# Kernel optimization log

Measured on AMD Instinct MI355X. Metric: run time of the kernel, lower is better.

The kernel has to match this reference:

```python
import jax, jax.numpy as jnp
import numpy as np

# Problem sizes
N = 131072      # total nodes (B graphs x 256 nodes)
E = 1048576     # total edges (avg degree 8)
V = 30000       # vocab
D = 128         # emb_size
H = 128         # hidden_size
T = 4           # num edge types; edge_to_id['ne'] == 0
L = 2           # num RGCN layers
B = 512         # num graphs in batch
PPG = 32        # predicate nodes per graph (uniform G_sizes)
IN_FEATS = D + 5  # emb + spo(3) + access(1) + pre_access(1)


def setup_inputs() -> dict:
    key = jax.random.key(0)
    ks = jax.random.split(key, 14)
    npg = N // B  # nodes per graph
    # predicate nodes: first PPG nodes of each graph (so G_sizes = [PPG]*B)
    pred_idx = (jnp.arange(B)[:, None] * npg + jnp.arange(PPG)[None, :]).reshape(-1)
    global_id = jax.random.randint(ks[0], (N,), 2, V)
    spo = jnp.zeros((N, 3), jnp.int32).at[pred_idx, 1].set(1)
    so = jax.random.randint(ks[1], (N, 2), 0, 2).astype(jnp.int32)
    notp = 1 - spo[:, 1]
    spo = spo.at[:, 0].set(so[:, 0] * notp).at[:, 2].set(so[:, 1] * notp)
    access = jax.random.randint(ks[2], (N, 1), 0, 5).astype(jnp.int32)
    pre_access = jax.random.randint(ks[3], (N, 1), 0, 5).astype(jnp.int32)
    src = jax.random.randint(ks[4], (E,), 0, N)
    dst = jax.random.randint(ks[5], (E,), 0, N)
    etype = jax.random.randint(ks[6], (E,), 0, T)
    norm = jax.random.uniform(ks[7], (E, 1), dtype=jnp.float32)
    # parameters
    emb_table = (0.02 * jax.random.normal(ks[8], (V, D), jnp.float32)).at[:2].set(0.0)
    W_t = 0.05 * jax.random.normal(ks[9], (IN_FEATS, H), jnp.float32)
    b_t = jnp.zeros((H,), jnp.float32)
    W_r = 0.05 * jax.random.normal(ks[10], (L, T, H, H), jnp.float32)
    b_r = jnp.zeros((L, H), jnp.float32)
    Wb = 0.05 * jax.random.normal(ks[11], (H, H), jnp.float32)
    bb = jnp.zeros((), jnp.float32)
    return {"emb_table": emb_table, "W_t": W_t, "b_t": b_t, "W_r": W_r,
            "b_r": b_r, "Wb": Wb, "bb": bb, "norm": norm,
            "global_id": global_id, "spo": spo, "access": access,
            "pre_access": pre_access, "src": src, "dst": dst,
            "etype": etype, "pred_idx": pred_idx}


def reference(emb_table, W_t, b_t, W_r, b_r, Wb, bb, norm,
              global_id, spo, access, pre_access, src, dst, etype, pred_idx):
    seg = lambda m, idx: jax.ops.segment_sum(m, idx, num_segments=N)
    # --- init_forward: send/recv over 'ne' edges, update only ne nodes with messages ---
    emb = emb_table[global_id]                                  # [N, D]
    ne = (etype == 0).astype(emb.dtype)[:, None]                # edge_to_id['ne'] == 0
    agg0 = seg(emb[src] * norm * ne, dst)                       # mailbox sum
    deg = seg(ne[:, 0], dst)
    is_ne = (spo[:, 0] + spo[:, 2]) > 0
    emb = jnp.where((is_ne & (deg > 0))[:, None], agg0, emb)
    # --- input projection ---
    h = jnp.concatenate([emb, spo.astype(emb.dtype), access.astype(emb.dtype),
                         pre_access.astype(emb.dtype)], axis=1) @ W_t + b_t  # [N, H]
    prev = h
    # --- RGCN layers: per-edge-type W, message = (h_src @ W_t) * norm, scatter-sum ---
    for l in range(L):
        agg = jnp.zeros((N, H), h.dtype)
        for t in range(T):
            mask_t = (etype == t).astype(h.dtype)[:, None]
            agg = agg + seg((h @ W_r[l, t])[src] * norm * mask_t, dst)
        h = jax.nn.relu(agg + b_r[l])
        if l != L - 1:  # residual, skipped on last layer as in source
            h = h + prev
            prev = h
    # --- predict: segment-mean pooling (equivalent to block-diag proj matmul) + bilinear ---
    hp = h[pred_idx].reshape(B, PPG, H)
    pool = hp.mean(axis=1)                                      # [B, H]
    out = jnp.einsum('bph,hk,bk->bp', hp, Wb, pool) + bb        # nn.Bilinear(H, H, 1)
    return jax.nn.log_softmax(out, axis=1).reshape(-1)          # per-graph log_softmax
```

## Files before the change

### kernel.cpp

```cpp
#include <hip/hip_runtime.h>
#include <hip/hip_bf16.h>

#define N_NODES 131072
#define N_EDGES 1048576
#define HID 128
#define NB 512
#define PPG 32
#define NTILES_D (N_NODES / 256)
#define KPROJ 160
#define KLAY  512

typedef short bf16x8 __attribute__((ext_vector_type(8)));
typedef float f32x4  __attribute__((ext_vector_type(4)));
typedef unsigned int u32x4 __attribute__((ext_vector_type(4)));

__device__ __forceinline__ float bf2f(unsigned short u) {
    return __uint_as_float(((unsigned int)u) << 16);
}
__device__ __forceinline__ unsigned short f2bf(float x) {
    unsigned int u = __float_as_uint(x);
    unsigned int r = ((u >> 16) & 1u) + 0x7fffu;
    return (unsigned short)((u + r) >> 16);
}
__device__ __forceinline__ unsigned int pack2(float a, float b) {
    return (unsigned int)f2bf(a) | ((unsigned int)f2bf(b) << 16);
}

__global__ void count_kernel(const int* __restrict__ dst, int* __restrict__ rp) {
    int e = blockIdx.x * blockDim.x + threadIdx.x;
    if (e >= N_EDGES) return;
    atomicAdd(rp + dst[e], 1);
}

__global__ void scan_tile_kernel(int* __restrict__ rp, int* __restrict__ tsum) {
    __shared__ int s[256];
    int g = blockIdx.x * 256 + threadIdx.x;
    int v = rp[g];
    s[threadIdx.x] = v;
    __syncthreads();
    for (int off = 1; off < 256; off <<= 1) {
        int tv = (threadIdx.x >= off) ? s[threadIdx.x - off] : 0;
        __syncthreads();
        s[threadIdx.x] += tv;
        __syncthreads();
    }
    rp[g] = s[threadIdx.x] - v;
    if (threadIdx.x == 255) tsum[blockIdx.x] = s[255];
}

__global__ void scan_tsum_kernel(int* __restrict__ tsum) {
    __shared__ int s[256];
    int t = threadIdx.x;
    int loc[2]; int sum = 0;
#pragma unroll
    for (int i = 0; i < 2; ++i) { loc[i] = tsum[t * 2 + i]; sum += loc[i]; }
    s[t] = sum;
    __syncthreads();
    for (int off = 1; off < 256; off <<= 1) {
        int tv = (t >= off) ? s[t - off] : 0;
        __syncthreads();
        s[t] += tv;
        __syncthreads();
    }
    int run = s[t] - sum;
#pragma unroll
    for (int i = 0; i < 2; ++i) { int v = loc[i]; tsum[t * 2 + i] = run; run += v; }
}

__global__ void scan_add_kernel(int* __restrict__ rp, const int* __restrict__ tsum) {
    int g = blockIdx.x * 256 + threadIdx.x;
    rp[g] += tsum[g >> 8];
}

__global__ void scatter_kernel(const int* __restrict__ src, const int* __restrict__ dst,
                               const int* __restrict__ etype, const float* __restrict__ norm,
                               int* __restrict__ rp, int2* __restrict__ erec) {
    int e = blockIdx.x * blockDim.x + threadIdx.x;
    if (e >= N_EDGES) return;
    int pos = atomicAdd(rp + dst[e], 1);
    erec[pos] = make_int2(src[e] | (etype[e] << 17), __float_as_int(norm[e]));
}

__global__ void wtrans_kernel(const float* __restrict__ W_t, const float* __restrict__ W_r,
                              unsigned short* __restrict__ WTp, unsigned short* __restrict__ WTl) {
    int u = blockIdx.x * 256 + threadIdx.x;
    if (u < 2560) {
        int c = u / 20, k0 = (u % 20) * 8;
#pragma unroll
        for (int j = 0; j < 8; ++j) {
            int k = k0 + j;
            float v = (k < 133) ? W_t[k * HID + c] : 0.f;
            WTp[c * KPROJ + k] = f2bf(v);
        }
    } else if (u < 2560 + 16384) {
        int v = u - 2560;
        int l = v / 8192; int rr = v % 8192;
        int c = rr / 64; int k0 = (rr % 64) * 8;
#pragma unroll
        for (int j = 0; j < 8; ++j) {
            int k = k0 + j; int t = k >> 7; int i = k & 127;
            float w = W_r[(((size_t)(l * 4 + t) * HID) + i) * HID + c];
            WTl[((size_t)l * HID + c) * KLAY + k] = f2bf(w);
        }
    }
}

__global__ __launch_bounds__(256) void prep_kernel(
        const int* __restrict__ rp, const int2* __restrict__ erec,
        const int* __restrict__ gid,
        const int* __restrict__ spo, const int* __restrict__ access,
        const int* __restrict__ pre, const float* __restrict__ emb,
        unsigned short* __restrict__ A0) {
    int wave = threadIdx.x >> 6, lane = threadIdx.x & 63;
    int n = blockIdx.x * 4 + wave;
    int g = lane >> 5, sl = lane & 31;
    int s0 = spo[n * 3], s1 = spo[n * 3 + 1], s2 = spo[n * 3 + 2];
    float a0 = 0.f, a1 = 0.f, a2 = 0.f, a3 = 0.f;
    int cnt = 0;
    bool isne = (s0 + s2) > 0;
    if (isne) {
        int rb = n ? rp[n - 1] : 0, re = rp[n];
        for (int i = rb + g; i < re; i += 2) {
            int2 er = erec[i];
            if (((er.x >> 17) & 3) == 0) {
                int s = er.x & 0x1FFFF;
                float nm = __int_as_float(er.y);
                float4 v = ((const float4*)(emb + (size_t)gid[s] * HID))[sl];
                a0 += v.x * nm; a1 += v.y * nm; a2 += v.z * nm; a3 += v.w * nm;
                cnt++;
            }
        }
        a0 += __shfl_xor(a0, 32, 64);
        a1 += __shfl_xor(a1, 32, 64);
        a2 += __shfl_xor(a2, 32, 64);
        a3 += __shfl_xor(a3, 32, 64);
        cnt += __shfl_xor(cnt, 32, 64);
    }
    if (!isne || cnt == 0) {
        if (g == 0) {
            float4 v = ((const float4*)(emb + (size_t)gid[n] * HID))[sl];
            a0 = v.x; a1 = v.y; a2 = v.z; a3 = v.w;
        }
    }
    unsigned int* row = (unsigned int*)(A0 + (size_t)n * KPROJ);
    if (g == 0) {
        uint2 o; o.x = pack2(a0, a1); o.y = pack2(a2, a3);
        *(uint2*)(row + sl * 2) = o;
    }
    if (lane < 16) {
        int c0 = 128 + lane * 2;
        float f0 = 0.f, f1 = 0.f;
        if (c0 == 128)      { f0 = (float)s0;      f1 = (float)s1; }
        else if (c0 == 130) { f0 = (float)s2;      f1 = (float)access[n]; }
        else if (c0 == 132) { f0 = (float)pre[n];  f1 = 0.f; }
        row[64 + lane] = pack2(f0, f1);
    }
}

__device__ __forceinline__ void stage_tile(const unsigned short* gbase, int ldK,
                                           int k0, int bk, unsigned short* lds,
                                           int wid, int lane) {
    int iters = bk >> 4;
    int sh = (bk == 128) ? 4 : ((bk == 64) ? 3 : 2);
    int msk = (1 << sh) - 1;
    for (int i = 0; i < iters; ++i) {
        int c = (i * 4 + wid) * 64 + lane;
        int row = c >> sh, cc = c & msk;
        int ccg = cc ^ (row & msk);
        const unsigned short* g = gbase + (size_t)row * ldK + k0 + ccg * 8;
        unsigned short* l = lds + (size_t)(i * 4 + wid) * 512;
        __builtin_amdgcn_global_load_lds(
            (const __attribute__((address_space(1))) void*)g,
            (__attribute__((address_space(3))) void*)l, 16, 0, 0);
    }
}

__global__ __launch_bounds__(256) void gemm_kernel(
        const unsigned short* __restrict__ A, int K,
        const unsigned short* __restrict__ WT, const float* __restrict__ bias,
        unsigned short* __restrict__ hb) {
    __shared__ unsigned short At[128 * 64];
    __shared__ unsigned short Bt[128 * 64];
    int tid = threadIdx.x;
    int base = blockIdx.x * 128;
    int wid = tid >> 6, lane = tid & 63;
    int wr = wid >> 1, wc = wid & 1;
    int lr = lane & 15, g16 = lane >> 4;
    f32x4 acc[4][4];
#pragma unroll
    for (int m = 0; m < 4; ++m)
#pragma unroll
        for (int n = 0; n < 4; ++n) { acc[m][n][0] = 0.f; acc[m][n][1] = 0.f; acc[m][n][2] = 0.f; acc[m][n][3] = 0.f; }
    const unsigned short* Abase = A + (size_t)base * K;
    for (int k0 = 0; k0 < K; k0 += 64) {
        int bk = K - k0; if (bk > 64) bk = 64;
        int swz = (bk == 64) ? 7 : 3;
        __syncthreads();
        stage_tile(Abase, K, k0, bk, At, wid, lane);
        stage_tile(WT,    K, k0, bk, Bt, wid, lane);
        __syncthreads();
        int ks = bk >> 5;
        for (int kk = 0; kk < ks; ++kk) {
            bf16x8 a[4], b[4];
            int cc = kk * 4 + g16;
#pragma unroll
            for (int m = 0; m < 4; ++m) {
                int ar = wr * 64 + m * 16 + lr;
                a[m] = *(const bf16x8*)&At[ar * bk + ((cc ^ (ar & swz)) << 3)];
            }
#pragma unroll
            for (int n = 0; n < 4; ++n) {
                int br = wc * 64 + n * 16 + lr;
                b[n] = *(const bf16x8*)&Bt[br * bk + ((cc ^ (br & swz)) << 3)];
            }
#pragma unroll
            for (int m = 0; m < 4; ++m)
#pragma unroll
                for (int n = 0; n < 4; ++n)
                    acc[m][n] = __builtin_amdgcn_mfma_f32_16x16x32_bf16(a[m], b[n], acc[m][n], 0, 0, 0);
        }
    }
    float bcol[4];
#pragma unroll
    for (int n = 0; n < 4; ++n) bcol[n] = bias[wc * 64 + n * 16 + lr];
    int r0g = (lane >> 4) * 4;
#pragma unroll
    for (int m = 0; m < 4; ++m) {
        int row = base + wr * 64 + m * 16 + r0g;
#pragma unroll
        for (int n = 0; n < 4; ++n) {
            int col = wc * 64 + n * 16 + lr;
#pragma unroll
            for (int r = 0; r < 4; ++r)
                hb[(size_t)(row + r) * HID + col] = f2bf(acc[m][n][r] + bcol[n]);
        }
    }
}

__global__ __launch_bounds__(256) void xt4_kernel(
        const unsigned short* __restrict__ hb,
        const unsigned short* __restrict__ WTlayer,
        unsigned short* __restrict__ XT) {
    __shared__ unsigned short Ah[128 * 128];
    __shared__ unsigned short Bt[128 * 128];
    int tid = threadIdx.x;
    int base = blockIdx.x * 128;
    int wid = tid >> 6, lane = tid & 63;
    int wr = wid >> 1, wc = wid & 1;
    int lr = lane & 15, g16 = lane >> 4;
    int r0g = (lane >> 4) * 4;

    stage_tile(hb + (size_t)base * HID, HID, 0, 128, Ah, wid, lane);
    stage_tile(WTlayer, KLAY, 0, 128, Bt, wid, lane);
    __syncthreads();

    for (int t = 0; t < 4; ++t) {
        f32x4 acc[4][4];
#pragma unroll
        for (int m = 0; m < 4; ++m)
#pragma unroll
            for (int n = 0; n < 4; ++n) { acc[m][n][0] = 0.f; acc[m][n][1] = 0.f; acc[m][n][2] = 0.f; acc[m][n][3] = 0.f; }
#pragma unroll
        for (int kk = 0; kk < 4; ++kk) {
            bf16x8 a[4], b[4];
            int cc = kk * 4 + g16;
#pragma unroll
            for (int m = 0; m < 4; ++m) {
                int ar = wr * 64 + m * 16 + lr;
                a[m] = *(const bf16x8*)&Ah[ar * 128 + ((cc ^ (ar & 15)) << 3)];
            }
#pragma unroll
            for (int n = 0; n < 4; ++n) {
                int br = wc * 64 + n * 16 + lr;
                b[n] = *(const bf16x8*)&Bt[br * 128 + ((cc ^ (br & 15)) << 3)];
            }
#pragma unroll
            for (int m = 0; m < 4; ++m)
#pragma unroll
                for (int n = 0; n < 4; ++n)
                    acc[m][n] = __builtin_amdgcn_mfma_f32_16x16x32_bf16(a[m], b[n], acc[m][n], 0, 0, 0);
        }
        unsigned short* XTt = XT + ((size_t)t << 17) * HID;
#pragma unroll
        for (int m = 0; m < 4; ++m) {
            int row = base + wr * 64 + m * 16 + r0g;
#pragma unroll
            for (int n = 0; n < 4; ++n) {
                int col = wc * 64 + n * 16 + lr;
#pragma unroll
                for (int r = 0; r < 4; ++r)
                    XTt[(size_t)(row + r) * HID + col] = f2bf(acc[m][n][r]);
            }
        }
        if (t < 3) {
            __syncthreads();
            stage_tile(WTlayer, KLAY, (t + 1) * HID, 128, Bt, wid, lane);
            __syncthreads();
        }
    }
}

__device__ __forceinline__ void acc8(float* a, u32x4 v, float nm) {
    a[0] = fmaf(bf2f((unsigned short)(v.x & 0xffffu)), nm, a[0]);
    a[1] = fmaf(bf2f((unsigned short)(v.x >> 16)),     nm, a[1]);
    a[2] = fmaf(bf2f((unsigned short)(v.y & 0xffffu)), nm, a[2]);
    a[3] = fmaf(bf2f((unsigned short)(v.y >> 16)),     nm, a[3]);
    a[4] = fmaf(bf2f((unsigned short)(v.z & 0xffffu)), nm, a[4]);
    a[5] = fmaf(bf2f((unsigned short)(v.z >> 16)),     nm, a[5]);
    a[6] = fmaf(bf2f((unsigned short)(v.w & 0xffffu)), nm, a[6]);
    a[7] = fmaf(bf2f((unsigned short)(v.w >> 16)),     nm, a[7]);
}

__global__ __launch_bounds__(256) void agg_kernel(
        const int* __restrict__ rp, const int2* __restrict__ erec,
        const unsigned short* __restrict__ XT, const float* __restrict__ bias,
        unsigned short* __restrict__ hb, int residual) {
    int wave = threadIdx.x >> 6, lane = threadIdx.x & 63;
    int d = blockIdx.x * 4 + wave;
    int g = lane >> 4, sl = lane & 15;
    int rb = d ? rp[d - 1] : 0;
    int re = rp[d];
    float a[8] = {0.f, 0.f, 0.f, 0.f, 0.f, 0.f, 0.f, 0.f};
    for (int i = rb + g; i < re; i += 4) {
        int2 er = erec[i];
        int st = er.x;
        float nm = __int_as_float(er.y);
        u32x4 v = *((const u32x4*)(XT + (size_t)(st & 0x7FFFF) * HID) + sl);
        acc8(a, v, nm);
    }
#pragma unroll
    for (int k = 0; k < 8; ++k) {
        a[k] += __shfl_xor(a[k], 16, 64);
        a[k] += __shfl_xor(a[k], 32, 64);
    }
    if (g == 0) {
        float r[8];
#pragma unroll
        for (int j = 0; j < 8; ++j) r[j] = fmaxf(a[j] + bias[sl * 8 + j], 0.f);
        unsigned short* hrow = hb + (size_t)d * HID;
        if (residual) {
            u32x4 hv = *((const u32x4*)hrow + sl);
            r[0] += bf2f((unsigned short)(hv.x & 0xffffu));
            r[1] += bf2f((unsigned short)(hv.x >> 16));
            r[2] += bf2f((unsigned short)(hv.y & 0xffffu));
            r[3] += bf2f((unsigned short)(hv.y >> 16));
            r[4] += bf2f((unsigned short)(hv.z & 0xffffu));
            r[5] += bf2f((unsigned short)(hv.z >> 16));
            r[6] += bf2f((unsigned short)(hv.w & 0xffffu));
            r[7] += bf2f((unsigned short)(hv.w >> 16));
        }
        u32x4 o;
        o.x = pack2(r[0], r[1]); o.y = pack2(r[2], r[3]);
        o.z = pack2(r[4], r[5]); o.w = pack2(r[6], r[7]);
        *((u32x4*)hrow + sl) = o;
    }
}

__global__ void predict_kernel(const unsigned short* __restrict__ hb,
                               const int* __restrict__ pred_idx,
                               const float* __restrict__ Wb, const float* __restrict__ bbp,
                               float* __restrict__ out) {
    int b = blockIdx.x;
    int tid = threadIdx.x;
    __shared__ float hp[PPG * HID];
    __shared__ float pool[HID];
    __shared__ float vv[HID];
    __shared__ float sc[PPG];
    __shared__ float lse;
    for (int k = tid; k < PPG * HID; k += 256) {
        int p = k >> 7, j = k & 127;
        int node = pred_idx[b * PPG + p];
        hp[k] = bf2f(hb[(size_t)node * HID + j]);
    }
    __syncthreads();
    if (tid < HID) {
        float s = 0.f;
        for (int p = 0; p < PPG; ++p) s += hp[p * HID + tid];
        pool[tid] = s * (1.0f / PPG);
    }
    __syncthreads();
    if (tid < HID) {
        float s = 0.f;
        for (int k = 0; k < HID; ++k) s += Wb[tid * HID + k] * pool[k];
        vv[tid] = s;
    }
    __syncthreads();
    if (tid < PPG) {
        float s = bbp[0];
        for (int j = 0; j < HID; ++j) s += hp[tid * HID + j] * vv[j];
        sc[tid] = s;
    }
    __syncthreads();
    if (tid == 0) {
        float m = -INFINITY;
        for (int p = 0; p < PPG; ++p) m = fmaxf(m, sc[p]);
        float se = 0.f;
        for (int p = 0; p < PPG; ++p) se += expf(sc[p] - m);
        lse = m + logf(se);
    }
    __syncthreads();
    if (tid < PPG) out[b * PPG + tid] = sc[tid] - lse;
}

extern "C" void kernel_launch(void* const* d_in, const int* in_sizes, int n_in,
                              void* d_out, int out_size, void* d_ws, size_t ws_size,
                              hipStream_t stream) {
    const float* emb_table  = (const float*)d_in[0];
    const float* W_t        = (const float*)d_in[1];
    const float* b_t        = (const float*)d_in[2];
    const float* W_r        = (const float*)d_in[3];
    const float* b_r        = (const float*)d_in[4];
    const float* Wb         = (const float*)d_in[5];
    const float* bb         = (const float*)d_in[6];
    const float* norm       = (const float*)d_in[7];
    const int*   global_id  = (const int*)d_in[8];
    const int*   spo        = (const int*)d_in[9];
    const int*   access     = (const int*)d_in[10];
    const int*   pre_access = (const int*)d_in[11];
    const int*   src        = (const int*)d_in[12];
    const int*   dst        = (const int*)d_in[13];
    const int*   etype      = (const int*)d_in[14];
    const int*   pred_idx   = (const int*)d_in[15];
    float* out = (float*)d_out;

    char* ws = (char*)d_ws;
    size_t off = 0;
    unsigned short* hb  = (unsigned short*)(ws + off); off += (size_t)N_NODES * HID * 2;
    unsigned short* XT  = (unsigned short*)(ws + off); off += (size_t)4 * N_NODES * HID * 2;
    int*   rp    = (int*)(ws + off);   off += (size_t)N_NODES * 4;
    int*   tsum  = (int*)(ws + off);   off += (size_t)NTILES_D * 4;
    int2*  erec  = (int2*)(ws + off);  off += (size_t)N_EDGES * 8;
    unsigned short* WTp = (unsigned short*)(ws + off); off += (size_t)HID * KPROJ * 2;
    unsigned short* WTl = (unsigned short*)(ws + off); off += (size_t)2 * HID * KLAY * 2;
    unsigned short* A0 = XT;

    hipMemsetAsync(rp, 0, (size_t)N_NODES * 4, stream);
    count_kernel<<<N_EDGES / 256, 256, 0, stream>>>(dst, rp);
    scan_tile_kernel<<<NTILES_D, 256, 0, stream>>>(rp, tsum);
    scan_tsum_kernel<<<1, 256, 0, stream>>>(tsum);
    scan_add_kernel<<<NTILES_D, 256, 0, stream>>>(rp, tsum);
    scatter_kernel<<<N_EDGES / 256, 256, 0, stream>>>(src, dst, etype, norm, rp, erec);

    wtrans_kernel<<<74, 256, 0, stream>>>(W_t, W_r, WTp, WTl);

    prep_kernel<<<N_NODES / 4, 256, 0, stream>>>(rp, erec, global_id, spo,
                                                 access, pre_access, emb_table, A0);
    gemm_kernel<<<N_NODES / 128, 256, 0, stream>>>(A0, KPROJ, WTp, b_t, hb);

    xt4_kernel<<<N_NODES / 128, 256, 0, stream>>>(hb, WTl, XT);
    agg_kernel<<<N_NODES / 4, 256, 0, stream>>>(rp, erec, XT, b_r, hb, 1);
    xt4_kernel<<<N_NODES / 128, 256, 0, stream>>>(hb, WTl + (size_t)HID * KLAY, XT);
    agg_kernel<<<N_NODES / 4, 256, 0, stream>>>(rp, erec, XT, b_r + HID, hb, 0);

    predict_kernel<<<NB, 256, 0, stream>>>(hb, pred_idx, Wb, bb, out);
}
```

Baseline: 509.7 us.

## Partition CSR edges by type, unroll gathers, read xt4 weights from global

The edge count and scatter now place type-0 edges first in each destination's CSR segment, using separate counters. This lets prep_kernel walk only the 'ne' edges without a per-edge type test. The scan output now serves as start offsets, so neighbouring kernels read rp[d] and rp[d+1]. The prep and agg gather loops are unrolled by two to keep more loads in flight. xt4_kernel keeps the A fragments in registers and loads B fragments straight from global memory instead of restaging LDS with barriers, which raises register pressure and global traffic. In exchange, scatter gains extra atomics and the memset clears more memory.

```diff
diff --git a/kernel.cpp b/kernel.cpp
--- a/kernel.cpp
+++ b/kernel.cpp
@@ -26,10 +26,13 @@
     return (unsigned int)f2bf(a) | ((unsigned int)f2bf(b) << 16);
 }
 
-__global__ void count_kernel(const int* __restrict__ dst, int* __restrict__ rp) {
+__global__ void count_kernel(const int* __restrict__ dst, const int* __restrict__ etype,
+                             int* __restrict__ rp, int* __restrict__ n0) {
     int e = blockIdx.x * blockDim.x + threadIdx.x;
     if (e >= N_EDGES) return;
-    atomicAdd(rp + dst[e], 1);
+    int d = dst[e];
+    atomicAdd(rp + d, 1);
+    if (etype[e] == 0) atomicAdd(n0 + d, 1);
 }
 
 __global__ void scan_tile_kernel(int* __restrict__ rp, int* __restrict__ tsum) {
@@ -74,11 +77,17 @@
 
 __global__ void scatter_kernel(const int* __restrict__ src, const int* __restrict__ dst,
                                const int* __restrict__ etype, const float* __restrict__ norm,
-                               int* __restrict__ rp, int2* __restrict__ erec) {
+                               const int* __restrict__ rp, const int* __restrict__ n0,
+                               int* __restrict__ c0, int* __restrict__ c1,
+                               int2* __restrict__ erec) {
     int e = blockIdx.x * blockDim.x + threadIdx.x;
     if (e >= N_EDGES) return;
-    int pos = atomicAdd(rp + dst[e], 1);
-    erec[pos] = make_int2(src[e] | (etype[e] << 17), __float_as_int(norm[e]));
+    int d = dst[e], t = etype[e];
+    int base = rp[d];
+    int pos;
+    if (t == 0) pos = base + atomicAdd(c0 + d, 1);
+    else        pos = base + n0[d] + atomicAdd(c1 + d, 1);
+    erec[pos] = make_int2(src[e] | (t << 17), __float_as_int(norm[e]));
 }
 
 __global__ void wtrans_kernel(const float* __restrict__ W_t, const float* __restrict__ W_r,
@@ -106,8 +115,8 @@
 }
 
 __global__ __launch_bounds__(256) void prep_kernel(
-        const int* __restrict__ rp, const int2* __restrict__ erec,
-        const int* __restrict__ gid,
+        const int* __restrict__ rp, const int* __restrict__ n0,
+        const int2* __restrict__ erec, const int* __restrict__ gid,
         const int* __restrict__ spo, const int* __restrict__ access,
         const int* __restrict__ pre, const float* __restrict__ emb,
         unsigned short* __restrict__ A0) {
@@ -116,31 +125,32 @@
     int g = lane >> 5, sl = lane & 31;
     int s0 = spo[n * 3], s1 = spo[n * 3 + 1], s2 = spo[n * 3 + 2];
     float a0 = 0.f, a1 = 0.f, a2 = 0.f, a3 = 0.f;
-    int cnt = 0;
-    bool isne = (s0 + s2) > 0;
-    if (isne) {
-        int rb = n ? rp[n - 1] : 0, re = rp[n];
-        for (int i = rb + g; i < re; i += 2) {
-            int2 er = erec[i];
-            if (((er.x >> 17) & 3) == 0) {
-                int s = er.x & 0x1FFFF;
-                float nm = __int_as_float(er.y);
-                float4 v = ((const float4*)(emb + (size_t)gid[s] * HID))[sl];
-                a0 += v.x * nm; a1 += v.y * nm; a2 += v.z * nm; a3 += v.w * nm;
-                cnt++;
-            }
+    int n0v = n0[n];
+    bool useagg = ((s0 + s2) > 0) && (n0v > 0);
+    if (useagg) {
+        int rb = rp[n], re = rb + n0v;
+        int i = rb + g;
+        for (; i + 2 < re; i += 4) {
+            int2 e0 = erec[i], e1 = erec[i + 2];
+            float nm0 = __int_as_float(e0.y), nm1 = __int_as_float(e1.y);
+            float4 v0 = ((const float4*)(emb + (size_t)gid[e0.x & 0x1FFFF] * HID))[sl];
+            float4 v1 = ((const float4*)(emb + (size_t)gid[e1.x & 0x1FFFF] * HID))[sl];
+            a0 += v0.x * nm0; a1 += v0.y * nm0; a2 += v0.z * nm0; a3 += v0.w * nm0;
+            a0 += v1.x * nm1; a1 += v1.y * nm1; a2 += v1.z * nm1; a3 += v1.w * nm1;
+        }
+        if (i < re) {
+            int2 e0 = erec[i];
+            float nm = __int_as_float(e0.y);
+            float4 v = ((const float4*)(emb + (size_t)gid[e0.x & 0x1FFFF] * HID))[sl];
+            a0 += v.x * nm; a1 += v.y * nm; a2 += v.z * nm; a3 += v.w * nm;
         }
         a0 += __shfl_xor(a0, 32, 64);
         a1 += __shfl_xor(a1, 32, 64);
         a2 += __shfl_xor(a2, 32, 64);
         a3 += __shfl_xor(a3, 32, 64);
-        cnt += __shfl_xor(cnt, 32, 64);
-    }
-    if (!isne || cnt == 0) {
-        if (g == 0) {
-            float4 v = ((const float4*)(emb + (size_t)gid[n] * HID))[sl];
-            a0 = v.x; a1 = v.y; a2 = v.z; a3 = v.w;
-        }
+    } else if (g == 0) {
+        float4 v = ((const float4*)(emb + (size_t)gid[n] * HID))[sl];
+        a0 = v.x; a1 = v.y; a2 = v.z; a3 = v.w;
     }
     unsigned int* row = (unsigned int*)(A0 + (size_t)n * KPROJ);
     if (g == 0) {
@@ -148,11 +158,11 @@
         *(uint2*)(row + sl * 2) = o;
     }
     if (lane < 16) {
-        int c0 = 128 + lane * 2;
+        int c0v = 128 + lane * 2;
         float f0 = 0.f, f1 = 0.f;
-        if (c0 == 128)      { f0 = (float)s0;      f1 = (float)s1; }
-        else if (c0 == 130) { f0 = (float)s2;      f1 = (float)access[n]; }
-        else if (c0 == 132) { f0 = (float)pre[n];  f1 = 0.f; }
+        if (c0v == 128)      { f0 = (float)s0;      f1 = (float)s1; }
+        else if (c0v == 130) { f0 = (float)s2;      f1 = (float)access[n]; }
+        else if (c0v == 132) { f0 = (float)pre[n];  f1 = 0.f; }
         row[64 + lane] = pack2(f0, f1);
     }
 }
@@ -242,17 +252,26 @@
         const unsigned short* __restrict__ WTlayer,
         unsigned short* __restrict__ XT) {
     __shared__ unsigned short Ah[128 * 128];
-    __shared__ unsigned short Bt[128 * 128];
     int tid = threadIdx.x;
     int base = blockIdx.x * 128;
     int wid = tid >> 6, lane = tid & 63;
     int wr = wid >> 1, wc = wid & 1;
     int lr = lane & 15, g16 = lane >> 4;
-    int r0g = (lane >> 4) * 4;
+    int r0g = g16 * 4;
 
     stage_tile(hb + (size_t)base * HID, HID, 0, 128, Ah, wid, lane);
-    stage_tile(WTlayer, KLAY, 0, 128, Bt, wid, lane);
-    __syncthreads();
+    __syncthreads();
+
+    bf16x8 a[4][4];
+#pragma unroll
+    for (int kk = 0; kk < 4; ++kk) {
+        int cc = kk * 4 + g16;
+#pragma unroll
+        for (int m = 0; m < 4; ++m) {
+            int ar = wr * 64 + m * 16 + lr;
+            a[kk][m] = *(const bf16x8*)&Ah[ar * 128 + ((cc ^ (ar & 15)) << 3)];
+        }
+    }
 
     for (int t = 0; t < 4; ++t) {
         f32x4 acc[4][4];
@@ -262,23 +281,18 @@
             for (int n = 0; n < 4; ++n) { acc[m][n][0] = 0.f; acc[m][n][1] = 0.f; acc[m][n][2] = 0.f; acc[m][n][3] = 0.f; }
 #pragma unroll
         for (int kk = 0; kk < 4; ++kk) {
-            bf16x8 a[4], b[4];
-            int cc = kk * 4 + g16;
-#pragma unroll
-            for (int m = 0; m < 4; ++m) {
-                int ar = wr * 64 + m * 16 + lr;
-                a[m] = *(const bf16x8*)&Ah[ar * 128 + ((cc ^ (ar & 15)) << 3)];
-            }
+            bf16x8 b[4];
 #pragma unroll
             for (int n = 0; n < 4; ++n) {
                 int br = wc * 64 + n * 16 + lr;
-                b[n] = *(const bf16x8*)&Bt[br * 128 + ((cc ^ (br & 15)) << 3)];
+                b[n] = *(const bf16x8*)(WTlayer + (size_t)br * KLAY + t * HID
+                                        + ((kk * 4 + g16) << 3));
             }
 #pragma unroll
             for (int m = 0; m < 4; ++m)
 #pragma unroll
                 for (int n = 0; n < 4; ++n)
-                    acc[m][n] = __builtin_amdgcn_mfma_f32_16x16x32_bf16(a[m], b[n], acc[m][n], 0, 0, 0);
+                    acc[m][n] = __builtin_amdgcn_mfma_f32_16x16x32_bf16(a[kk][m], b[n], acc[m][n], 0, 0, 0);
         }
         unsigned short* XTt = XT + ((size_t)t << 17) * HID;
 #pragma unroll
@@ -291,11 +305,6 @@
                 for (int r = 0; r < 4; ++r)
                     XTt[(size_t)(row + r) * HID + col] = f2bf(acc[m][n][r]);
             }
-        }
-        if (t < 3) {
-            __syncthreads();
-            stage_tile(WTlayer, KLAY, (t + 1) * HID, 128, Bt, wid, lane);
-            __syncthreads();
         }
     }
 }
@@ -318,15 +327,22 @@
     int wave = threadIdx.x >> 6, lane = threadIdx.x & 63;
     int d = blockIdx.x * 4 + wave;
     int g = lane >> 4, sl = lane & 15;
-    int rb = d ? rp[d - 1] : 0;
-    int re = rp[d];
+    int rb = rp[d];
+    int re = (d == N_NODES - 1) ? N_EDGES : rp[d + 1];
     float a[8] = {0.f, 0.f, 0.f, 0.f, 0.f, 0.f, 0.f, 0.f};
-    for (int i = rb + g; i < re; i += 4) {
-        int2 er = erec[i];
-        int st = er.x;
-        float nm = __int_as_float(er.y);
-        u32x4 v = *((const u32x4*)(XT + (size_t)(st & 0x7FFFF) * HID) + sl);
-        acc8(a, v, nm);
+    int i = rb + g;
+    for (; i + 4 < re; i += 8) {
+        int2 e0 = erec[i];
+        int2 e1 = erec[i + 4];
+        u32x4 v0 = *((const u32x4*)(XT + (size_t)(e0.x & 0x7FFFF) * HID) + sl);
+        u32x4 v1 = *((const u32x4*)(XT + (size_t)(e1.x & 0x7FFFF) * HID) + sl);
+        acc8(a, v0, __int_as_float(e0.y));
+        acc8(a, v1, __int_as_float(e1.y));
+    }
+    if (i < re) {
+        int2 e0 = erec[i];
+        u32x4 v0 = *((const u32x4*)(XT + (size_t)(e0.x & 0x7FFFF) * HID) + sl);
+        acc8(a, v0, __int_as_float(e0.y));
     }
 #pragma unroll
     for (int k = 0; k < 8; ++k) {
@@ -428,22 +444,26 @@
     unsigned short* hb  = (unsigned short*)(ws + off); off += (size_t)N_NODES * HID * 2;
     unsigned short* XT  = (unsigned short*)(ws + off); off += (size_t)4 * N_NODES * HID * 2;
     int*   rp    = (int*)(ws + off);   off += (size_t)N_NODES * 4;
+    int*   n0    = (int*)(ws + off);   off += (size_t)N_NODES * 4;
+    int*   c0    = (int*)(ws + off);   off += (size_t)N_NODES * 4;
+    int*   c1    = (int*)(ws + off);   off += (size_t)N_NODES * 4;
     int*   tsum  = (int*)(ws + off);   off += (size_t)NTILES_D * 4;
     int2*  erec  = (int2*)(ws + off);  off += (size_t)N_EDGES * 8;
     unsigned short* WTp = (unsigned short*)(ws + off); off += (size_t)HID * KPROJ * 2;
     unsigned short* WTl = (unsigned short*)(ws + off); off += (size_t)2 * HID * KLAY * 2;
     unsigned short* A0 = XT;
 
-    hipMemsetAsync(rp, 0, (size_t)N_NODES * 4, stream);
-    count_kernel<<<N_EDGES / 256, 256, 0, stream>>>(dst, rp);
+    hipMemsetAsync(rp, 0, (size_t)4 * N_NODES * 4, stream);
+    count_kernel<<<N_EDGES / 256, 256, 0, stream>>>(dst, etype, rp, n0);
     scan_tile_kernel<<<NTILES_D, 256, 0, stream>>>(rp, tsum);
     scan_tsum_kernel<<<1, 256, 0, stream>>>(tsum);
     scan_add_kernel<<<NTILES_D, 256, 0, stream>>>(rp, tsum);
-    scatter_kernel<<<N_EDGES / 256, 256, 0, stream>>>(src, dst, etype, norm, rp, erec);
+    scatter_kernel<<<N_EDGES / 256, 256, 0, stream>>>(src, dst, etype, norm,
+                                                      rp, n0, c0, c1, erec);
 
     wtrans_kernel<<<74, 256, 0, stream>>>(W_t, W_r, WTp, WTl);
 
-    prep_kernel<<<N_NODES / 4, 256, 0, stream>>>(rp, erec, global_id, spo,
+    prep_kernel<<<N_NODES / 4, 256, 0, stream>>>(rp, n0, erec, global_id, spo,
                                                  access, pre_access, emb_table, A0);
     gemm_kernel<<<N_NODES / 128, 256, 0, stream>>>(A0, KPROJ, WTp, b_t, hb);
 
```

New measurement: 515.8 us. No clear change (+1.2%).
